# Optimization experiments

Measured on AMD Instinct MI355X. Metric: run time of the kernel, lower is better.

The kernel has to match this reference:

```python
import jax, jax.numpy as jnp
import numpy as np

H = 128          # input hidden dim
HID = 128        # expert hidden width
OUT = 128        # out_channels
NR = 8           # n_routed
NS = 2           # n_shared
RDIM = 16        # router feature dim


def setup_inputs() -> dict:
    key = jax.random.key(0)
    ks = jax.random.split(key, 11)
    s = 0.05
    x = jax.random.normal(ks[0], (2, 32, 32, 32, H), dtype=jnp.float32)
    # router params
    Wr1 = jax.random.normal(ks[1], (H, RDIM), dtype=jnp.float32) * s
    br1 = jnp.zeros((RDIM,), dtype=jnp.float32)
    Wr2 = jax.random.normal(ks[2], (RDIM, NR), dtype=jnp.float32) * s
    br2 = jnp.zeros((NR,), dtype=jnp.float32)
    # routed expert params, stacked on leading expert axis
    We1 = jax.random.normal(ks[3], (NR, H, HID), dtype=jnp.float32) * s
    be1 = jnp.zeros((NR, HID), dtype=jnp.float32)
    We2 = jax.random.normal(ks[4], (NR, HID, OUT), dtype=jnp.float32) * s
    be2 = jnp.zeros((NR, OUT), dtype=jnp.float32)
    # shared expert params
    Ws1 = jax.random.normal(ks[5], (NS, H, HID), dtype=jnp.float32) * s
    bs1 = jnp.zeros((NS, HID), dtype=jnp.float32)
    Ws2 = jax.random.normal(ks[6], (NS, HID, OUT), dtype=jnp.float32) * s
    bs2 = jnp.zeros((NS, OUT), dtype=jnp.float32)
    return dict(x=x, Wr1=Wr1, br1=br1, Wr2=Wr2, br2=br2,
                We1=We1, be1=be1, We2=We2, be2=be2,
                Ws1=Ws1, bs1=bs1, Ws2=Ws2, bs2=bs2)


def reference(x, Wr1, br1, Wr2, br2, We1, be1, We2, be2, Ws1, bs1, Ws2, bs2):
    # router: Dense(16) -> relu -> Dense(n_routed) -> softmax
    rf = jax.nn.relu(jnp.einsum('...h,hr->...r', x, Wr1) + br1)
    logits = jnp.einsum('...r,re->...e', rf, Wr2) + br2
    gate = jax.nn.softmax(logits, axis=-1)                      # [..., NR]
    threshold = 1.0 / NR
    mask = (gate > threshold).astype(gate.dtype)
    mg = gate * mask
    mg = mg / (jnp.sum(mg, axis=-1, keepdims=True) + 1e-8)
    # routed experts (batched over expert axis e): Dense -> gelu(tanh) -> Dense
    hr = jax.nn.gelu(jnp.einsum('...h,ehd->...ed', x, We1) + be1)   # [..., NR, HID]
    ro = jnp.einsum('...ed,edo->...eo', hr, We2) + be2              # [..., NR, OUT]
    routed_agg = jnp.einsum('...eo,...e->...o', ro, mg)
    # shared experts summed
    hs = jax.nn.gelu(jnp.einsum('...h,ehd->...ed', x, Ws1) + bs1)   # [..., NS, HID]
    so = jnp.einsum('...ed,edo->...eo', hs, Ws2) + bs2              # [..., NS, OUT]
    shared_agg = jnp.sum(so, axis=-2)
    return routed_agg + shared_agg
```

## Files before the change

kernel.cpp:

```cpp
#include <hip/hip_runtime.h>
#include <hip/hip_bf16.h>

typedef __bf16 bf16x8 __attribute__((ext_vector_type(8)));
typedef float  f32x16 __attribute__((ext_vector_type(16)));
typedef float  f32x4  __attribute__((ext_vector_type(4)));
typedef float  f32x2  __attribute__((ext_vector_type(2)));

static __device__ __forceinline__ f32x16 mfma32(bf16x8 a, bf16x8 b, f32x16 c) {
    return __builtin_amdgcn_mfma_f32_32x32x16_bf16(a, b, c, 0, 0, 0);
}

#define GELU_C1 2.30220820f
#define GELU_C2 0.10294324f

__global__ __launch_bounds__(256) void pack_kernel(
    const float* __restrict__ We1, const float* __restrict__ be1,
    const float* __restrict__ Ws1, const float* __restrict__ bs1,
    const float* __restrict__ We2, const float* __restrict__ Ws2,
    __bf16* __restrict__ w1p, __bf16* __restrict__ w2p)
{
    int tid = blockIdx.x * 256 + threadIdx.x;
    if (tid < 23040) {
        int l  = tid & 63;
        int ks = (tid >> 6) % 9;
        int nt = (tid / 576) & 3;
        int e  = tid / 2304;
        const float* src = (e < 8) ? (We1 + e * 16384) : (Ws1 + (e - 8) * 16384);
        const float* bia = (e < 8) ? (be1 + e * 128)   : (bs1 + (e - 8) * 128);
        int n = nt * 32 + (l & 31);
        int kb = ks * 16 + (l >> 5) * 8;
        bf16x8 v;
        #pragma unroll
        for (int j = 0; j < 8; ++j) {
            int k = kb + j;
            float f = (k < 128) ? src[k * 128 + n] : ((k == 128) ? bia[n] : 0.f);
            v[j] = (__bf16)f;
        }
        *(bf16x8*)(w1p + (size_t)tid * 8) = v;
    } else if (tid < 43520) {
        int t2 = tid - 23040;
        int l  = t2 & 63;
        int ks = (t2 >> 6) & 7;
        int ot = (t2 / 512) & 3;
        int e  = t2 / 2048;
        const float* src = (e < 8) ? (We2 + e * 16384) : (Ws2 + (e - 8) * 16384);
        int o  = ot * 32 + (l & 31);
        int lh = l >> 5;
        bf16x8 v;
        #pragma unroll
        for (int j = 0; j < 8; ++j) {
            int hid = 16 * ks + 8 * (j >> 2) + 4 * lh + (j & 3);
            v[j] = (__bf16)src[hid * 128 + o];
        }
        *(bf16x8*)(w2p + (size_t)t2 * 8) = v;
    }
}

__global__ __launch_bounds__(64) void router_kernel(
    const float* __restrict__ x,
    const float* __restrict__ Wr1, const float* __restrict__ br1,
    const float* __restrict__ Wr2, const float* __restrict__ br2,
    float* __restrict__ mg)
{
    __shared__ __align__(16) float xs[64 * 132];
    int t = threadIdx.x;
    size_t base = (size_t)blockIdx.x * 64 * 128;
    #pragma unroll 4
    for (int i = 0; i < 32; ++i) {
        int idx = i * 64 + t;
        f32x4 v = *(const f32x4*)(x + base + (size_t)idx * 4);
        int m = (idx * 4) >> 7;
        int c = (idx * 4) & 127;
        *(f32x4*)&xs[m * 132 + c] = v;
    }
    __syncthreads();

    const f32x4* xr = (const f32x4*)(xs + t * 132);
    double rf[16];
    #pragma unroll
    for (int r = 0; r < 16; ++r) rf[r] = (double)br1[r];
    for (int c = 0; c < 32; ++c) {
        f32x4 xv4 = xr[c];
        #pragma unroll
        for (int q = 0; q < 4; ++q) {
            double xv = (double)xv4[q];
            int k = c * 4 + q;
            #pragma unroll
            for (int r = 0; r < 16; ++r)
                rf[r] = fma(xv, (double)Wr1[k * 16 + r], rf[r]);
        }
    }
    #pragma unroll
    for (int r = 0; r < 16; ++r) rf[r] = rf[r] > 0.0 ? rf[r] : 0.0;
    double lg[8];
    #pragma unroll
    for (int j = 0; j < 8; ++j) lg[j] = (double)br2[j];
    #pragma unroll
    for (int r = 0; r < 16; ++r) {
        double rv = rf[r];
        #pragma unroll
        for (int j = 0; j < 8; ++j)
            lg[j] = fma(rv, (double)Wr2[r * 8 + j], lg[j]);
    }
    double mx = lg[0];
    #pragma unroll
    for (int j = 1; j < 8; ++j) mx = lg[j] > mx ? lg[j] : mx;
    double ex[8]; double s = 0.0;
    #pragma unroll
    for (int j = 0; j < 8; ++j) { ex[j] = exp(lg[j] - mx); s += ex[j]; }
    double mv[8]; double ms = 0.0;
    #pragma unroll
    for (int j = 0; j < 8; ++j) {
        double g = ex[j] / s;
        double m = (g > 0.125) ? g : 0.0;
        mv[j] = m; ms += m;
    }
    double inv = 1.0 / (ms + 1e-8);
    int tok = blockIdx.x * 64 + t;
    f32x4 o0, o1;
    o0[0]=(float)(mv[0]*inv); o0[1]=(float)(mv[1]*inv);
    o0[2]=(float)(mv[2]*inv); o0[3]=(float)(mv[3]*inv);
    o1[0]=(float)(mv[4]*inv); o1[1]=(float)(mv[5]*inv);
    o1[2]=(float)(mv[6]*inv); o1[3]=(float)(mv[7]*inv);
    f32x4* op = (f32x4*)(mg + (size_t)tok * 8);
    op[0] = o0; op[1] = o1;
}

__global__ __launch_bounds__(256, 2) void moe_main_kernel(
    const float* __restrict__ x, const float* __restrict__ mg,
    const __bf16* __restrict__ w1p, const __bf16* __restrict__ w2p,
    const float* __restrict__ be2, const float* __restrict__ bs2,
    float* __restrict__ out)
{
    __shared__ __align__(16) char lds[32768];
    __bf16* Xp = (__bf16*)lds;
    float*  Red = (float*)lds;

    const int t    = threadIdx.x;
    const int lane = t & 63;
    const int wave = t >> 6;
    const int l31  = lane & 31;
    const int lh   = lane >> 5;
    const int mt   = wave >> 1;
    const int h    = wave & 1;
    const int tok0 = blockIdx.x * 64;

    #pragma unroll
    for (int i = 0; i < 4; ++i) {
        int g = i * 256 + t;
        int m = g >> 4;
        int c = g & 15;
        const f32x4* sp = (const f32x4*)(x + (size_t)(tok0 + m) * 128 + c * 8);
        f32x4 va = sp[0], vb = sp[1];
        bf16x8 v;
        v[0]=(__bf16)va[0]; v[1]=(__bf16)va[1]; v[2]=(__bf16)va[2]; v[3]=(__bf16)va[3];
        v[4]=(__bf16)vb[0]; v[5]=(__bf16)vb[1]; v[6]=(__bf16)vb[2]; v[7]=(__bf16)vb[3];
        *(bf16x8*)&Xp[(((m >> 5) * 9 + (c >> 1)) * 64 + (c & 1) * 32 + (m & 31)) * 8] = v;
    }
    if (t < 128) {
        int mtx = t >> 6, l = t & 63;
        bf16x8 v;
        #pragma unroll
        for (int j = 0; j < 8; ++j) v[j] = (__bf16)0.f;
        if (l < 32) v[0] = (__bf16)1.0f;
        *(bf16x8*)&Xp[((mtx * 9 + 8) * 64 + l) * 8] = v;
    }
    __syncthreads();

    const float* mgr = mg + (size_t)(tok0 + 32 * mt + l31) * 8;
    f32x4 ga4 = *(const f32x4*)mgr;
    f32x4 gb4 = *(const f32x4*)(mgr + 4);
    float gte[8] = {ga4[0], ga4[1], ga4[2], ga4[3], gb4[0], gb4[1], gb4[2], gb4[3]};

    f32x16 acc[4];
    #pragma unroll
    for (int ot = 0; ot < 4; ++ot)
        #pragma unroll
        for (int i = 0; i < 16; ++i) acc[ot][i] = 0.f;

    const bf16x8* w1v = (const bf16x8*)w1p;
    const bf16x8* w2v = (const bf16x8*)w2p;

    #pragma unroll 1
    for (int e = 0; e < 10; ++e) {
        const bf16x8* wap = w1v + ((size_t)(e * 4 + 2 * h) * 9) * 64 + lane;
        bf16x8 wa[9], wb[9];
        #pragma unroll
        for (int ks = 0; ks < 9; ++ks) { wa[ks] = wap[ks * 64]; wb[ks] = wap[(9 + ks) * 64]; }

        f32x16 a1[2];
        #pragma unroll
        for (int n2 = 0; n2 < 2; ++n2)
            #pragma unroll
            for (int i = 0; i < 16; ++i) a1[n2][i] = 0.f;

        #pragma unroll
        for (int ks = 0; ks < 9; ++ks) {
            bf16x8 xb = *(const bf16x8*)&Xp[((mt * 9 + ks) * 64 + lane) * 8];
            a1[0] = mfma32(wa[ks], xb, a1[0]);
            a1[1] = mfma32(wb[ks], xb, a1[1]);
        }

        const bf16x8* wBp = w2v + ((size_t)(e * 4) * 8 + 4 * h) * 64 + lane;
        bf16x8 wB[4][4];
        #pragma unroll
        for (int ot = 0; ot < 4; ++ot)
            #pragma unroll
            for (int kq = 0; kq < 4; ++kq)
                wB[ot][kq] = wBp[(ot * 8 + kq) * 64];

        const float gv = (e < 8) ? gte[e] : 1.0f;

        #pragma unroll
        for (int n2 = 0; n2 < 2; ++n2) {
            #pragma unroll
            for (int b = 0; b < 2; ++b) {
                bf16x8 fr;
                #pragma unroll
                for (int jp = 0; jp < 4; ++jp) {
                    f32x2 hh; hh[0] = a1[n2][8 * b + 2 * jp]; hh[1] = a1[n2][8 * b + 2 * jp + 1];
                    f32x2 tt = hh * hh;
                    f32x2 pp;
                    pp[0] = fmaf(tt[0], -GELU_C2, -GELU_C1);
                    pp[1] = fmaf(tt[1], -GELU_C2, -GELU_C1);
                    f32x2 mm = hh * pp;
                    float e0 = __builtin_amdgcn_exp2f(mm[0]);
                    float e1 = __builtin_amdgcn_exp2f(mm[1]);
                    float q0 = __builtin_amdgcn_rcpf(1.f + e0);
                    float q1 = __builtin_amdgcn_rcpf(1.f + e1);
                    f32x2 gg; gg[0] = hh[0] * q0 * gv; gg[1] = hh[1] * q1 * gv;
                    fr[2 * jp]     = (__bf16)gg[0];
                    fr[2 * jp + 1] = (__bf16)gg[1];
                }
                int kq = 2 * n2 + b;
                acc[0] = mfma32(fr, wB[0][kq], acc[0]);
                acc[1] = mfma32(fr, wB[1][kq], acc[1]);
                acc[2] = mfma32(fr, wB[2][kq], acc[2]);
                acc[3] = mfma32(fr, wB[3][kq], acc[3]);
            }
        }
    }

    __syncthreads();
    if (h == 1) {
        #pragma unroll
        for (int ot = 0; ot < 4; ++ot)
            #pragma unroll
            for (int r = 0; r < 16; ++r)
                Red[((mt * 4 + ot) * 16 + r) * 64 + lane] = acc[ot][r];
    }
    __syncthreads();
    if (h == 0) {
        float be2c[4][8], bsc[4];
        #pragma unroll
        for (int ot = 0; ot < 4; ++ot) {
            int o = 32 * ot + l31;
            bsc[ot] = bs2[o] + bs2[128 + o];
            #pragma unroll
            for (int ee = 0; ee < 8; ++ee) be2c[ot][ee] = be2[ee * 128 + o];
        }
        const float* mgb = mg + (size_t)(tok0 + 32 * mt) * 8;
        #pragma unroll
        for (int r = 0; r < 16; ++r) {
            int mrow = (r & 3) + 8 * (r >> 2) + 4 * lh;
            f32x4 g0 = *(const f32x4*)&mgb[mrow * 8];
            f32x4 g1 = *(const f32x4*)&mgb[mrow * 8 + 4];
            size_t orow = (size_t)(tok0 + 32 * mt + mrow) * 128;
            #pragma unroll
            for (int ot = 0; ot < 4; ++ot) {
                float b = bsc[ot];
                #pragma unroll
                for (int ee = 0; ee < 4; ++ee) b = fmaf(g0[ee], be2c[ot][ee], b);
                #pragma unroll
                for (int ee = 0; ee < 4; ++ee) b = fmaf(g1[ee], be2c[ot][4 + ee], b);
                float v = acc[ot][r] + Red[((mt * 4 + ot) * 16 + r) * 64 + lane] + b;
                out[orow + 32 * ot + l31] = v;
            }
        }
    }
}

extern "C" void kernel_launch(void* const* d_in, const int* in_sizes, int n_in,
                              void* d_out, int out_size, void* d_ws, size_t ws_size,
                              hipStream_t stream)
{
    const float* x   = (const float*)d_in[0];
    const float* Wr1 = (const float*)d_in[1];
    const float* br1 = (const float*)d_in[2];
    const float* Wr2 = (const float*)d_in[3];
    const float* br2 = (const float*)d_in[4];
    const float* We1 = (const float*)d_in[5];
    const float* be1 = (const float*)d_in[6];
    const float* We2 = (const float*)d_in[7];
    const float* be2 = (const float*)d_in[8];
    const float* Ws1 = (const float*)d_in[9];
    const float* bs1 = (const float*)d_in[10];
    const float* Ws2 = (const float*)d_in[11];
    const float* bs2 = (const float*)d_in[12];

    __bf16* w1p = (__bf16*)d_ws;
    __bf16* w2p = (__bf16*)((char*)d_ws + 368640);
    float*  mg  = (float*)((char*)d_ws + 696320);

    pack_kernel<<<170, 256, 0, stream>>>(We1, be1, Ws1, bs1, We2, Ws2, w1p, w2p);
    router_kernel<<<1024, 64, 0, stream>>>(x, Wr1, br1, Wr2, br2, mg);
    moe_main_kernel<<<1024, 256, 0, stream>>>(x, mg, w1p, w2p, be2, bs2,
                                              (float*)d_out);
}
```

Measured before the change: 197.0 us.

## Fuse router computation into main MoE kernel via shared-memory staging

```diff
diff --git a/kernel.cpp b/kernel.cpp
--- a/kernel.cpp
+++ b/kernel.cpp
@@ -56,84 +56,19 @@
     }
 }
 
-__global__ __launch_bounds__(64) void router_kernel(
+__global__ __launch_bounds__(256, 2) void moe_main_kernel(
     const float* __restrict__ x,
     const float* __restrict__ Wr1, const float* __restrict__ br1,
     const float* __restrict__ Wr2, const float* __restrict__ br2,
-    float* __restrict__ mg)
-{
-    __shared__ __align__(16) float xs[64 * 132];
-    int t = threadIdx.x;
-    size_t base = (size_t)blockIdx.x * 64 * 128;
-    #pragma unroll 4
-    for (int i = 0; i < 32; ++i) {
-        int idx = i * 64 + t;
-        f32x4 v = *(const f32x4*)(x + base + (size_t)idx * 4);
-        int m = (idx * 4) >> 7;
-        int c = (idx * 4) & 127;
-        *(f32x4*)&xs[m * 132 + c] = v;
-    }
-    __syncthreads();
-
-    const f32x4* xr = (const f32x4*)(xs + t * 132);
-    double rf[16];
-    #pragma unroll
-    for (int r = 0; r < 16; ++r) rf[r] = (double)br1[r];
-    for (int c = 0; c < 32; ++c) {
-        f32x4 xv4 = xr[c];
-        #pragma unroll
-        for (int q = 0; q < 4; ++q) {
-            double xv = (double)xv4[q];
-            int k = c * 4 + q;
-            #pragma unroll
-            for (int r = 0; r < 16; ++r)
-                rf[r] = fma(xv, (double)Wr1[k * 16 + r], rf[r]);
-        }
-    }
-    #pragma unroll
-    for (int r = 0; r < 16; ++r) rf[r] = rf[r] > 0.0 ? rf[r] : 0.0;
-    double lg[8];
-    #pragma unroll
-    for (int j = 0; j < 8; ++j) lg[j] = (double)br2[j];
-    #pragma unroll
-    for (int r = 0; r < 16; ++r) {
-        double rv = rf[r];
-        #pragma unroll
-        for (int j = 0; j < 8; ++j)
-            lg[j] = fma(rv, (double)Wr2[r * 8 + j], lg[j]);
-    }
-    double mx = lg[0];
-    #pragma unroll
-    for (int j = 1; j < 8; ++j) mx = lg[j] > mx ? lg[j] : mx;
-    double ex[8]; double s = 0.0;
-    #pragma unroll
-    for (int j = 0; j < 8; ++j) { ex[j] = exp(lg[j] - mx); s += ex[j]; }
-    double mv[8]; double ms = 0.0;
-    #pragma unroll
-    for (int j = 0; j < 8; ++j) {
-        double g = ex[j] / s;
-        double m = (g > 0.125) ? g : 0.0;
-        mv[j] = m; ms += m;
-    }
-    double inv = 1.0 / (ms + 1e-8);
-    int tok = blockIdx.x * 64 + t;
-    f32x4 o0, o1;
-    o0[0]=(float)(mv[0]*inv); o0[1]=(float)(mv[1]*inv);
-    o0[2]=(float)(mv[2]*inv); o0[3]=(float)(mv[3]*inv);
-    o1[0]=(float)(mv[4]*inv); o1[1]=(float)(mv[5]*inv);
-    o1[2]=(float)(mv[6]*inv); o1[3]=(float)(mv[7]*inv);
-    f32x4* op = (f32x4*)(mg + (size_t)tok * 8);
-    op[0] = o0; op[1] = o1;
-}
-
-__global__ __launch_bounds__(256, 2) void moe_main_kernel(
-    const float* __restrict__ x, const float* __restrict__ mg,
     const __bf16* __restrict__ w1p, const __bf16* __restrict__ w2p,
     const float* __restrict__ be2, const float* __restrict__ bs2,
     float* __restrict__ out)
 {
-    __shared__ __align__(16) char lds[32768];
-    __bf16* Xp = (__bf16*)lds;
+    __shared__ __align__(16) char lds[62464];
+    float*  xs  = (float*)lds;
+    __bf16* Xp  = (__bf16*)(lds + 33792);
+    double* rfs = (double*)(lds + 33792 + 18432);
+    float*  mgs = (float*)(lds + 33792 + 18432 + 8192);
     float*  Red = (float*)lds;
 
     const int t    = threadIdx.x;
@@ -152,6 +87,8 @@
         int c = g & 15;
         const f32x4* sp = (const f32x4*)(x + (size_t)(tok0 + m) * 128 + c * 8);
         f32x4 va = sp[0], vb = sp[1];
+        *(f32x4*)&xs[m * 132 + c * 8]     = va;
+        *(f32x4*)&xs[m * 132 + c * 8 + 4] = vb;
         bf16x8 v;
         v[0]=(__bf16)va[0]; v[1]=(__bf16)va[1]; v[2]=(__bf16)va[2]; v[3]=(__bf16)va[3];
         v[4]=(__bf16)vb[0]; v[5]=(__bf16)vb[1]; v[6]=(__bf16)vb[2]; v[7]=(__bf16)vb[3];
@@ -167,7 +104,61 @@
     }
     __syncthreads();
 
-    const float* mgr = mg + (size_t)(tok0 + 32 * mt + l31) * 8;
+    {
+        const int tok = t & 63;
+        const int rq  = (t >> 6) * 4;
+        double rf4[4];
+        #pragma unroll
+        for (int j = 0; j < 4; ++j) rf4[j] = (double)br1[rq + j];
+        const f32x4* xr = (const f32x4*)(xs + tok * 132);
+        for (int c = 0; c < 32; ++c) {
+            f32x4 xv4 = xr[c];
+            #pragma unroll
+            for (int q = 0; q < 4; ++q) {
+                double xv = (double)xv4[q];
+                int k = c * 4 + q;
+                #pragma unroll
+                for (int j = 0; j < 4; ++j)
+                    rf4[j] = fma(xv, (double)Wr1[k * 16 + rq + j], rf4[j]);
+            }
+        }
+        #pragma unroll
+        for (int j = 0; j < 4; ++j)
+            rfs[tok * 16 + rq + j] = rf4[j] > 0.0 ? rf4[j] : 0.0;
+    }
+    __syncthreads();
+
+    if (t < 64) {
+        double lg[8];
+        #pragma unroll
+        for (int j = 0; j < 8; ++j) lg[j] = (double)br2[j];
+        #pragma unroll
+        for (int r = 0; r < 16; ++r) {
+            double rv = rfs[t * 16 + r];
+            #pragma unroll
+            for (int j = 0; j < 8; ++j)
+                lg[j] = fma(rv, (double)Wr2[r * 8 + j], lg[j]);
+        }
+        double mx = lg[0];
+        #pragma unroll
+        for (int j = 1; j < 8; ++j) mx = lg[j] > mx ? lg[j] : mx;
+        double ex[8]; double s = 0.0;
+        #pragma unroll
+        for (int j = 0; j < 8; ++j) { ex[j] = exp(lg[j] - mx); s += ex[j]; }
+        double mv[8]; double ms = 0.0;
+        #pragma unroll
+        for (int j = 0; j < 8; ++j) {
+            double g = ex[j] / s;
+            double m = (g > 0.125) ? g : 0.0;
+            mv[j] = m; ms += m;
+        }
+        double inv = 1.0 / (ms + 1e-8);
+        #pragma unroll
+        for (int j = 0; j < 8; ++j) mgs[t * 8 + j] = (float)(mv[j] * inv);
+    }
+    __syncthreads();
+
+    const float* mgr = mgs + (32 * mt + l31) * 8;
     f32x4 ga4 = *(const f32x4*)mgr;
     f32x4 gb4 = *(const f32x4*)(mgr + 4);
     float gte[8] = {ga4[0], ga4[1], ga4[2], ga4[3], gb4[0], gb4[1], gb4[2], gb4[3]};
@@ -188,6 +179,14 @@
         #pragma unroll
         for (int ks = 0; ks < 9; ++ks) { wa[ks] = wap[ks * 64]; wb[ks] = wap[(9 + ks) * 64]; }
 
+        const bf16x8* wBp = w2v + ((size_t)(e * 4) * 8 + 4 * h) * 64 + lane;
+        bf16x8 wB[4][4];
+        #pragma unroll
+        for (int ot = 0; ot < 4; ++ot)
+            #pragma unroll
+            for (int kq = 0; kq < 4; ++kq)
+                wB[ot][kq] = wBp[(ot * 8 + kq) * 64];
+
         f32x16 a1[2];
         #pragma unroll
         for (int n2 = 0; n2 < 2; ++n2)
@@ -200,14 +199,6 @@
             a1[0] = mfma32(wa[ks], xb, a1[0]);
             a1[1] = mfma32(wb[ks], xb, a1[1]);
         }
-
-        const bf16x8* wBp = w2v + ((size_t)(e * 4) * 8 + 4 * h) * 64 + lane;
-        bf16x8 wB[4][4];
-        #pragma unroll
-        for (int ot = 0; ot < 4; ++ot)
-            #pragma unroll
-            for (int kq = 0; kq < 4; ++kq)
-                wB[ot][kq] = wBp[(ot * 8 + kq) * 64];
 
         const float gv = (e < 8) ? gte[e] : 1.0f;
 
@@ -259,7 +250,7 @@
             #pragma unroll
             for (int ee = 0; ee < 8; ++ee) be2c[ot][ee] = be2[ee * 128 + o];
         }
-        const float* mgb = mg + (size_t)(tok0 + 32 * mt) * 8;
+        const float* mgb = mgs + (32 * mt) * 8;
         #pragma unroll
         for (int r = 0; r < 16; ++r) {
             int mrow = (r & 3) + 8 * (r >> 2) + 4 * lh;
@@ -300,10 +291,8 @@
 
     __bf16* w1p = (__bf16*)d_ws;
     __bf16* w2p = (__bf16*)((char*)d_ws + 368640);
-    float*  mg  = (float*)((char*)d_ws + 696320);
 
     pack_kernel<<<170, 256, 0, stream>>>(We1, be1, Ws1, bs1, We2, Ws2, w1p, w2p);
-    router_kernel<<<1024, 64, 0, stream>>>(x, Wr1, br1, Wr2, br2, mg);
-    moe_main_kernel<<<1024, 256, 0, stream>>>(x, mg, w1p, w2p, be2, bs2,
-                                              (float*)d_out);
-}
+    moe_main_kernel<<<1024, 256, 0, stream>>>(x, Wr1, br1, Wr2, br2,
+                                              w1p, w2p, be2, bs2, (float*)d_out);
+}
```

Result: no change. 200.1 us (+1.6%).
